# Optimization experiments

Measured on AMD Instinct MI355X. Metric: run time of the kernel, lower is better.

The kernel has to match this reference:

```python
import jax, jax.numpy as jnp
import numpy as np

N = 50000
E = 600000
D = 128
BN_EPS = 1e-5
GIN_EPS = 0.0  # init_eps=0, not learned


def setup_inputs() -> dict:
    key = jax.random.key(0)
    ks = jax.random.split(key, 8)
    x = jax.random.normal(ks[0], (N, D), dtype=jnp.float32)
    edge_index = jax.random.randint(ks[1], (2, E), 0, N, dtype=jnp.int64)
    s = 1.0 / np.sqrt(D)
    w1 = jax.random.uniform(ks[2], (D, D), jnp.float32, -s, s)
    b1 = jax.random.uniform(ks[3], (D,), jnp.float32, -s, s)
    w2 = jax.random.uniform(ks[4], (D, D), jnp.float32, -s, s)
    b2 = jax.random.uniform(ks[5], (D,), jnp.float32, -s, s)
    gamma = jnp.ones((D,), jnp.float32)
    beta = jnp.zeros((D,), jnp.float32)
    return {"x": x, "edge_index": edge_index, "w1": w1, "b1": b1,
            "w2": w2, "b2": b2, "gamma": gamma, "beta": beta}


def reference(x, edge_index, w1, b1, w2, b2, gamma, beta):
    src, dst = edge_index[0], edge_index[1]
    # GINConv sum aggregation: out[i] = sum_{(j,i) in E} x[j]
    agg = jax.ops.segment_sum(x[src], dst, num_segments=N)  # [N, D]
    h = (1.0 + GIN_EPS) * x + agg
    # 2-layer MLP (Linear-ReLU-Linear)
    h = jax.nn.relu(h @ w1 + b1)
    h = h @ w2 + b2
    # training-mode BatchNorm over nodes (biased variance)
    mean = jnp.mean(h, axis=0)
    var = jnp.var(h, axis=0)
    h = (h - mean) * jax.lax.rsqrt(var + BN_EPS) * gamma + beta
    h = jax.nn.relu(h)
    # residual (in_dim == out_dim); dropout p=0.0 -> identity
    return x + h
```

## Files before the change

### kernel.cpp

```cpp
#include <hip/hip_runtime.h>

#define NN 50000
#define EE 600000
#define DD 128
#define MAXDEG 64
#define NSLICE 32
#define EPT 4

typedef __attribute__((ext_vector_type(8))) short short8;
typedef __attribute__((ext_vector_type(4))) float f32x4;

static __device__ __forceinline__ unsigned short f2bf(float f) {
    unsigned int u = __float_as_uint(f);
    u += 0x7FFF + ((u >> 16) & 1);
    return (unsigned short)(u >> 16);
}
static __device__ __forceinline__ float bflo(unsigned int u) {
    return __uint_as_float(u << 16);
}
static __device__ __forceinline__ float bfhi(unsigned int u) {
    return __uint_as_float(u & 0xFFFF0000u);
}


__global__ __launch_bounds__(256) void k_prep(const float* __restrict__ w1,
                                              const float* __restrict__ w2,
                                              const float* __restrict__ x,
                                              const int* __restrict__ ei,
                                              int* __restrict__ cursor,
                                              unsigned short* __restrict__ srcPad,
                                              unsigned short* __restrict__ wt,
                                              unsigned int* __restrict__ xb) {
    int tid = blockIdx.x * 256 + threadIdx.x;
    if (tid < EE / EPT) {
        #pragma unroll
        for (int i = 0; i < EPT; ++i) {
            int e = tid + i * (EE / EPT);
            int s = ei[e];
            int d = ei[EE + e];
            int pos = atomicAdd(&cursor[d], 1);
            if (pos < MAXDEG) srcPad[(d << 6) + pos] = (unsigned short)s;
        }
    }
    if (tid < 32768) {
        int w = tid >> 14, idx = tid & 16383;
        int k = idx >> 7, n = idx & 127;
        const float* src = w ? w2 : w1;
        wt[w * 16384 + n * 128 + k] = f2bf(src[k * 128 + n]);
    }
    int xi = tid - 32768;
    if (xi >= 0 && xi < NN * DD / 2) {
        float2 v = ((const float2*)x)[xi];
        xb[xi] = (unsigned int)f2bf(v.x) | ((unsigned int)f2bf(v.y) << 16);
    }
}


__global__ __launch_bounds__(256) void k_agg(const unsigned int* __restrict__ xb,
                                             const int* __restrict__ cursor,
                                             const unsigned short* __restrict__ srcPad,
                                             unsigned int* __restrict__ h0) {
    int wave = (blockIdx.x * blockDim.x + threadIdx.x) >> 6;
    int lane = threadIdx.x & 63;
    if (wave >= NN) return;
    int cnt = cursor[wave];
    if (cnt > MAXDEG) cnt = MAXDEG;
    int sv = srcPad[(wave << 6) + lane];
    unsigned int self = xb[(wave << 6) + lane];
    float ax = bflo(self), ay = bfhi(self);
    int j = 0;
    for (; j + 8 <= cnt; j += 8) {
        int a0 = __shfl(sv, j, 64),     a1 = __shfl(sv, j + 1, 64);
        int a2 = __shfl(sv, j + 2, 64), a3 = __shfl(sv, j + 3, 64);
        int a4 = __shfl(sv, j + 4, 64), a5 = __shfl(sv, j + 5, 64);
        int a6 = __shfl(sv, j + 6, 64), a7 = __shfl(sv, j + 7, 64);
        unsigned int u0 = xb[(a0 << 6) + lane], u1 = xb[(a1 << 6) + lane];
        unsigned int u2 = xb[(a2 << 6) + lane], u3 = xb[(a3 << 6) + lane];
        unsigned int u4 = xb[(a4 << 6) + lane], u5 = xb[(a5 << 6) + lane];
        unsigned int u6 = xb[(a6 << 6) + lane], u7 = xb[(a7 << 6) + lane];
        ax += bflo(u0) + bflo(u1) + bflo(u2) + bflo(u3)
            + bflo(u4) + bflo(u5) + bflo(u6) + bflo(u7);
        ay += bfhi(u0) + bfhi(u1) + bfhi(u2) + bfhi(u3)
            + bfhi(u4) + bfhi(u5) + bfhi(u6) + bfhi(u7);
    }
    for (; j + 4 <= cnt; j += 4) {
        int a0 = __shfl(sv, j, 64),     a1 = __shfl(sv, j + 1, 64);
        int a2 = __shfl(sv, j + 2, 64), a3 = __shfl(sv, j + 3, 64);
        unsigned int u0 = xb[(a0 << 6) + lane], u1 = xb[(a1 << 6) + lane];
        unsigned int u2 = xb[(a2 << 6) + lane], u3 = xb[(a3 << 6) + lane];
        ax += bflo(u0) + bflo(u1) + bflo(u2) + bflo(u3);
        ay += bfhi(u0) + bfhi(u1) + bfhi(u2) + bfhi(u3);
    }
    for (; j < cnt; ++j) {
        int s = __shfl(sv, j, 64);
        unsigned int u = xb[(s << 6) + lane];
        ax += bflo(u);
        ay += bfhi(u);
    }
    h0[(wave << 6) + lane] = (unsigned int)f2bf(ax) | ((unsigned int)f2bf(ay) << 16);
}


__global__ __launch_bounds__(256) void k_gemm(const unsigned short* __restrict__ A,
                                              const unsigned short* __restrict__ W,
                                              const float* __restrict__ bias,
                                              unsigned short* __restrict__ Cb,
                                              float* __restrict__ priv,
                                              int relu) {
    int wave = (blockIdx.x * 256 + threadIdx.x) >> 6;
    int lane = threadIdx.x & 63;
    int m = lane & 15, quad = lane >> 4;
    int row0 = wave * 32;
    if (row0 >= NN) return;

    short8 af[2][4];
    #pragma unroll
    for (int mt = 0; mt < 2; ++mt) {
        int gr = row0 + mt * 16 + m;
        #pragma unroll
        for (int kc = 0; kc < 4; ++kc)
            af[mt][kc] = (gr < NN) ? *(const short8*)&A[gr * 128 + kc * 32 + quad * 8]
                                   : (short8)0;
    }

    f32x4 acc[2][8];
    #pragma unroll
    for (int mt = 0; mt < 2; ++mt)
        #pragma unroll
        for (int i = 0; i < 8; ++i) acc[mt][i] = (f32x4)0.f;

    #pragma unroll
    for (int h = 0; h < 2; ++h) {
        short8 wf[4][4];
        #pragma unroll
        for (int nt = 0; nt < 4; ++nt)
            #pragma unroll
            for (int kc = 0; kc < 4; ++kc)
                wf[nt][kc] = *(const short8*)&W[(h * 64 + nt * 16 + m) * 128 + kc * 32 + quad * 8];
        #pragma unroll
        for (int kc = 0; kc < 4; ++kc)
            #pragma unroll
            for (int nt = 0; nt < 4; ++nt) {
                acc[0][h * 4 + nt] = __builtin_amdgcn_mfma_f32_16x16x32_bf16(af[0][kc], wf[nt][kc], acc[0][h * 4 + nt], 0, 0, 0);
                acc[1][h * 4 + nt] = __builtin_amdgcn_mfma_f32_16x16x32_bf16(af[1][kc], wf[nt][kc], acc[1][h * 4 + nt], 0, 0, 0);
            }
    }

    if (relu) {
        #pragma unroll
        for (int nt = 0; nt < 8; ++nt) {
            int col = nt * 16 + m;
            float bv = bias[col];
            #pragma unroll
            for (int mt = 0; mt < 2; ++mt)
                #pragma unroll
                for (int r = 0; r < 4; ++r) {
                    int gr = row0 + mt * 16 + quad * 4 + r;
                    if (gr < NN) Cb[gr * 128 + col] = f2bf(fmaxf(acc[mt][nt][r] + bv, 0.f));
                }
        }
    } else {
        float* myslice = priv + (wave & (NSLICE - 1)) * 2 * DD;
        #pragma unroll
        for (int nt = 0; nt < 8; ++nt) {
            int col = nt * 16 + m;
            float bv = bias[col];
            float s = 0.f, sq = 0.f;
            #pragma unroll
            for (int mt = 0; mt < 2; ++mt)
                #pragma unroll
                for (int r = 0; r < 4; ++r) {
                    int gr = row0 + mt * 16 + quad * 4 + r;
                    if (gr < NN) {
                        float v = acc[mt][nt][r] + bv;
                        Cb[gr * 128 + col] = f2bf(v);
                        s += v;
                        sq += v * v;
                    }
                }
            s  += __shfl_down(s, 32, 64);  sq += __shfl_down(sq, 32, 64);
            s  += __shfl_down(s, 16, 64);  sq += __shfl_down(sq, 16, 64);
            if (quad == 0) {
                atomicAdd(&myslice[col], s);
                atomicAdd(&myslice[DD + col], sq);
            }
        }
    }
}


__global__ __launch_bounds__(256) void k_final(const float* __restrict__ x,
                                               const unsigned int* __restrict__ h2,
                                               float* __restrict__ out,
                                               const float* __restrict__ priv,
                                               const float* __restrict__ gamma,
                                               const float* __restrict__ beta) {
    __shared__ float ssc[DD], ssh[DD];
    int t = threadIdx.x;
    if (t < DD) {
        float s = 0.f, sq = 0.f;
        #pragma unroll
        for (int sl = 0; sl < NSLICE; ++sl) {
            s  += priv[sl * 2 * DD + t];
            sq += priv[sl * 2 * DD + DD + t];
        }
        float mean = s * (1.0f / NN);
        float var = fmaxf(sq * (1.0f / NN) - mean * mean, 0.f);
        float sc = gamma[t] * rsqrtf(var + 1e-5f);
        ssc[t] = sc;
        ssh[t] = beta[t] - mean * sc;
    }
    __syncthreads();
    #pragma unroll
    for (int u = 0; u < 4; ++u) {
        int idx = blockIdx.x * 1024 + u * 256 + t;
        if (idx >= NN * DD / 4) return;
        int c0 = (idx & 31) * 4;
        unsigned int p0 = h2[2 * idx];
        unsigned int p1 = h2[2 * idx + 1];
        float4 xv = ((const float4*)x)[idx];
        float4 o;
        o.x = xv.x + fmaxf(fmaf(bflo(p0), ssc[c0 + 0], ssh[c0 + 0]), 0.f);
        o.y = xv.y + fmaxf(fmaf(bfhi(p0), ssc[c0 + 1], ssh[c0 + 1]), 0.f);
        o.z = xv.z + fmaxf(fmaf(bflo(p1), ssc[c0 + 2], ssh[c0 + 2]), 0.f);
        o.w = xv.w + fmaxf(fmaf(bfhi(p1), ssc[c0 + 3], ssh[c0 + 3]), 0.f);
        ((float4*)out)[idx] = o;
    }
}

extern "C" void kernel_launch(void* const* d_in, const int* in_sizes, int n_in,
                              void* d_out, int out_size, void* d_ws, size_t ws_size,
                              hipStream_t stream) {
    (void)in_sizes; (void)n_in; (void)out_size; (void)ws_size;
    const float* x     = (const float*)d_in[0];
    const int*   ei    = (const int*)d_in[1];
    const float* w1    = (const float*)d_in[2];
    const float* b1    = (const float*)d_in[3];
    const float* w2    = (const float*)d_in[4];
    const float* b2    = (const float*)d_in[5];
    const float* gamma = (const float*)d_in[6];
    const float* beta  = (const float*)d_in[7];
    float* out = (float*)d_out;

    char* wsb = (char*)d_ws;
    int*            cursor = (int*)(wsb);
    unsigned short* srcPad = (unsigned short*)(wsb + 0x40000);
    unsigned int*   xb     = (unsigned int*)(wsb + 0x680000);
    unsigned short* h1b    = (unsigned short*)xb;
    unsigned int*   h0w    = (unsigned int*)(wsb + 0x1300000);
    unsigned short* h0b    = (unsigned short*)h0w;
    unsigned short* h2b    = (unsigned short*)h0w;
    unsigned int*   h2w    = (unsigned int*)h0w;
    unsigned short* wt     = (unsigned short*)(wsb + 0x1F80000);
    float*          priv   = (float*)(wsb + 0x1FA0000);

    (void)hipMemsetAsync(cursor, 0, NN * sizeof(int), stream);
    (void)hipMemsetAsync(priv, 0, NSLICE * 2 * DD * sizeof(float), stream);

    k_prep<<<(32768 + NN * DD / 2 + 255) / 256, 256, 0, stream>>>(w1, w2, x, ei, cursor, srcPad, wt, xb);
    k_agg<<<(NN * 64 + 255) / 256, 256, 0, stream>>>(xb, cursor, srcPad, h0w);
    k_gemm<<<(NN + 127) / 128, 256, 0, stream>>>(h0b, wt, b1, h1b, nullptr, 1);
    k_gemm<<<(NN + 127) / 128, 256, 0, stream>>>(h1b, wt + 16384, b2, h2b, priv, 0);
    k_final<<<(NN * DD / 4 + 1023) / 1024, 256, 0, stream>>>(x, h2w, out, priv, gamma, beta);
}
```

Baseline: 192.9 us.

## Fuse the two MLP GEMMs into one kernel with the hidden tile kept in LDS

Replaces the two separate GEMM launches with one k_mlp kernel. Each block computes 64 rows of the first linear plus ReLU, stores the bf16 hidden tile in padded shared memory, then runs the second GEMM and the BatchNorm statistics from it. This removes the global write and re-read of the intermediate activation and one launch. It also merges the two memsets into one by moving priv next to cursor, and raises EPT to 8. In exchange, each wave now handles 16 rows instead of 32, so every W fragment loaded feeds fewer MFMAs.

```diff
diff --git a/kernel.cpp b/kernel.cpp
--- a/kernel.cpp
+++ b/kernel.cpp
@@ -3,9 +3,10 @@
 #define NN 50000
 #define EE 600000
 #define DD 128
+#define LDSTR 136
 #define MAXDEG 64
 #define NSLICE 32
-#define EPT 4
+#define EPT 8
 
 typedef __attribute__((ext_vector_type(8))) short short8;
 typedef __attribute__((ext_vector_type(4))) float f32x4;
@@ -101,34 +102,28 @@
 }
 
 
-__global__ __launch_bounds__(256) void k_gemm(const unsigned short* __restrict__ A,
-                                              const unsigned short* __restrict__ W,
-                                              const float* __restrict__ bias,
-                                              unsigned short* __restrict__ Cb,
-                                              float* __restrict__ priv,
-                                              int relu) {
-    int wave = (blockIdx.x * 256 + threadIdx.x) >> 6;
-    int lane = threadIdx.x & 63;
+__global__ __launch_bounds__(256) void k_mlp(const unsigned short* A,
+                                             const unsigned short* __restrict__ wt,
+                                             const float* __restrict__ b1,
+                                             const float* __restrict__ b2,
+                                             unsigned short* C,
+                                             float* __restrict__ priv) {
+    __shared__ __align__(16) unsigned short H1s[64 * LDSTR];
+    int t = threadIdx.x;
+    int lane = t & 63, wid = t >> 6;
     int m = lane & 15, quad = lane >> 4;
-    int row0 = wave * 32;
-    if (row0 >= NN) return;
-
-    short8 af[2][4];
-    #pragma unroll
-    for (int mt = 0; mt < 2; ++mt) {
-        int gr = row0 + mt * 16 + m;
-        #pragma unroll
-        for (int kc = 0; kc < 4; ++kc)
-            af[mt][kc] = (gr < NN) ? *(const short8*)&A[gr * 128 + kc * 32 + quad * 8]
-                                   : (short8)0;
-    }
-
-    f32x4 acc[2][8];
-    #pragma unroll
-    for (int mt = 0; mt < 2; ++mt)
-        #pragma unroll
-        for (int i = 0; i < 8; ++i) acc[mt][i] = (f32x4)0.f;
-
+    int row0 = blockIdx.x * 64 + wid * 16;
+
+    int gra = row0 + m;
+    short8 af[4];
+    #pragma unroll
+    for (int kc = 0; kc < 4; ++kc)
+        af[kc] = (gra < NN) ? *(const short8*)&A[gra * 128 + kc * 32 + quad * 8]
+                            : (short8)0;
+
+    f32x4 acc[8];
+    #pragma unroll
+    for (int i = 0; i < 8; ++i) acc[i] = (f32x4)0.f;
     #pragma unroll
     for (int h = 0; h < 2; ++h) {
         short8 wf[4][4];
@@ -136,54 +131,67 @@
         for (int nt = 0; nt < 4; ++nt)
             #pragma unroll
             for (int kc = 0; kc < 4; ++kc)
-                wf[nt][kc] = *(const short8*)&W[(h * 64 + nt * 16 + m) * 128 + kc * 32 + quad * 8];
+                wf[nt][kc] = *(const short8*)&wt[(h * 64 + nt * 16 + m) * 128 + kc * 32 + quad * 8];
         #pragma unroll
         for (int kc = 0; kc < 4; ++kc)
             #pragma unroll
-            for (int nt = 0; nt < 4; ++nt) {
-                acc[0][h * 4 + nt] = __builtin_amdgcn_mfma_f32_16x16x32_bf16(af[0][kc], wf[nt][kc], acc[0][h * 4 + nt], 0, 0, 0);
-                acc[1][h * 4 + nt] = __builtin_amdgcn_mfma_f32_16x16x32_bf16(af[1][kc], wf[nt][kc], acc[1][h * 4 + nt], 0, 0, 0);
+            for (int nt = 0; nt < 4; ++nt)
+                acc[h * 4 + nt] = __builtin_amdgcn_mfma_f32_16x16x32_bf16(af[kc], wf[nt][kc], acc[h * 4 + nt], 0, 0, 0);
+    }
+
+    #pragma unroll
+    for (int nt = 0; nt < 8; ++nt) {
+        int col = nt * 16 + m;
+        float bv = b1[col];
+        #pragma unroll
+        for (int r = 0; r < 4; ++r)
+            H1s[(wid * 16 + quad * 4 + r) * LDSTR + col] = f2bf(fmaxf(acc[nt][r] + bv, 0.f));
+    }
+    __syncthreads();
+
+    short8 af2[4];
+    #pragma unroll
+    for (int kc = 0; kc < 4; ++kc)
+        af2[kc] = *(const short8*)&H1s[(wid * 16 + m) * LDSTR + kc * 32 + quad * 8];
+
+    #pragma unroll
+    for (int i = 0; i < 8; ++i) acc[i] = (f32x4)0.f;
+    #pragma unroll
+    for (int h = 0; h < 2; ++h) {
+        short8 wf[4][4];
+        #pragma unroll
+        for (int nt = 0; nt < 4; ++nt)
+            #pragma unroll
+            for (int kc = 0; kc < 4; ++kc)
+                wf[nt][kc] = *(const short8*)&wt[16384 + (h * 64 + nt * 16 + m) * 128 + kc * 32 + quad * 8];
+        #pragma unroll
+        for (int kc = 0; kc < 4; ++kc)
+            #pragma unroll
+            for (int nt = 0; nt < 4; ++nt)
+                acc[h * 4 + nt] = __builtin_amdgcn_mfma_f32_16x16x32_bf16(af2[kc], wf[nt][kc], acc[h * 4 + nt], 0, 0, 0);
+    }
+
+    float* myslice = priv + ((blockIdx.x * 4 + wid) & (NSLICE - 1)) * 2 * DD;
+    #pragma unroll
+    for (int nt = 0; nt < 8; ++nt) {
+        int col = nt * 16 + m;
+        float bv = b2[col];
+        float s = 0.f, sq = 0.f;
+        #pragma unroll
+        for (int r = 0; r < 4; ++r) {
+            int gr = row0 + quad * 4 + r;
+            if (gr < NN) {
+                float v = acc[nt][r] + bv;
+                C[gr * 128 + col] = f2bf(v);
+                s += v;
+                sq += v * v;
             }
-    }
-
-    if (relu) {
-        #pragma unroll
-        for (int nt = 0; nt < 8; ++nt) {
-            int col = nt * 16 + m;
-            float bv = bias[col];
-            #pragma unroll
-            for (int mt = 0; mt < 2; ++mt)
-                #pragma unroll
-                for (int r = 0; r < 4; ++r) {
-                    int gr = row0 + mt * 16 + quad * 4 + r;
-                    if (gr < NN) Cb[gr * 128 + col] = f2bf(fmaxf(acc[mt][nt][r] + bv, 0.f));
-                }
-        }
-    } else {
-        float* myslice = priv + (wave & (NSLICE - 1)) * 2 * DD;
-        #pragma unroll
-        for (int nt = 0; nt < 8; ++nt) {
-            int col = nt * 16 + m;
-            float bv = bias[col];
-            float s = 0.f, sq = 0.f;
-            #pragma unroll
-            for (int mt = 0; mt < 2; ++mt)
-                #pragma unroll
-                for (int r = 0; r < 4; ++r) {
-                    int gr = row0 + mt * 16 + quad * 4 + r;
-                    if (gr < NN) {
-                        float v = acc[mt][nt][r] + bv;
-                        Cb[gr * 128 + col] = f2bf(v);
-                        s += v;
-                        sq += v * v;
-                    }
-                }
-            s  += __shfl_down(s, 32, 64);  sq += __shfl_down(sq, 32, 64);
-            s  += __shfl_down(s, 16, 64);  sq += __shfl_down(sq, 16, 64);
-            if (quad == 0) {
-                atomicAdd(&myslice[col], s);
-                atomicAdd(&myslice[DD + col], sq);
-            }
+        }
+        s  += __shfl_down(s, 32, 64);  sq += __shfl_down(sq, 32, 64);
+        s  += __shfl_down(s, 16, 64);  sq += __shfl_down(sq, 16, 64);
+        if (quad == 0) {
+            atomicAdd(&myslice[col], s);
+            atomicAdd(&myslice[DD + col], sq);
         }
     }
 }
@@ -244,22 +252,19 @@
 
     char* wsb = (char*)d_ws;
     int*            cursor = (int*)(wsb);
+    float*          priv   = (float*)(wsb + 0x31000);
     unsigned short* srcPad = (unsigned short*)(wsb + 0x40000);
     unsigned int*   xb     = (unsigned int*)(wsb + 0x680000);
-    unsigned short* h1b    = (unsigned short*)xb;
     unsigned int*   h0w    = (unsigned int*)(wsb + 0x1300000);
     unsigned short* h0b    = (unsigned short*)h0w;
     unsigned short* h2b    = (unsigned short*)h0w;
     unsigned int*   h2w    = (unsigned int*)h0w;
     unsigned short* wt     = (unsigned short*)(wsb + 0x1F80000);
-    float*          priv   = (float*)(wsb + 0x1FA0000);
-
-    (void)hipMemsetAsync(cursor, 0, NN * sizeof(int), stream);
-    (void)hipMemsetAsync(priv, 0, NSLICE * 2 * DD * sizeof(float), stream);
+
+    (void)hipMemsetAsync(wsb, 0, 0x39000, stream);
 
     k_prep<<<(32768 + NN * DD / 2 + 255) / 256, 256, 0, stream>>>(w1, w2, x, ei, cursor, srcPad, wt, xb);
     k_agg<<<(NN * 64 + 255) / 256, 256, 0, stream>>>(xb, cursor, srcPad, h0w);
-    k_gemm<<<(NN + 127) / 128, 256, 0, stream>>>(h0b, wt, b1, h1b, nullptr, 1);
-    k_gemm<<<(NN + 127) / 128, 256, 0, stream>>>(h1b, wt + 16384, b2, h2b, priv, 0);
+    k_mlp<<<(NN + 63) / 64, 256, 0, stream>>>(h0b, wt, b1, b2, h2b, priv);
     k_final<<<(NN * DD / 4 + 1023) / 1024, 256, 0, stream>>>(x, h2w, out, priv, gamma, beta);
 }
```

Result: slower. 199.8 us (+3.6%).

## Fuse all stages into one cooperative persistent kernel with grid syncs

Applied to the files above, without the earlier changes.

Replaces the memset plus five kernel launches with a single cooperative kernel that runs every stage (zeroing, CSR build, bf16 conversion, aggregation, both GEMMs, BatchNorm finalize) in grid-stride loops separated by grid.sync(). The aim is to remove launch and inter-kernel gaps. In exchange the stages run on a capped persistent grid, which may reduce parallelism and latency hiding, and each grid barrier has its own cost. Intermediate buffers are no longer aliased, and the old multi-kernel path is kept as a fallback.

```diff
diff --git a/kernel.cpp b/kernel.cpp
--- a/kernel.cpp
+++ b/kernel.cpp
@@ -1,11 +1,14 @@
 #include <hip/hip_runtime.h>
+#include <hip/hip_cooperative_groups.h>
+
+namespace cg = cooperative_groups;
 
 #define NN 50000
 #define EE 600000
 #define DD 128
 #define MAXDEG 64
 #define NSLICE 32
-#define EPT 4
+#define EPT 8
 
 typedef __attribute__((ext_vector_type(8))) short short8;
 typedef __attribute__((ext_vector_type(4))) float f32x4;
@@ -23,50 +26,96 @@
 }
 
 
-__global__ __launch_bounds__(256) void k_prep(const float* __restrict__ w1,
-                                              const float* __restrict__ w2,
-                                              const float* __restrict__ x,
-                                              const int* __restrict__ ei,
-                                              int* __restrict__ cursor,
-                                              unsigned short* __restrict__ srcPad,
-                                              unsigned short* __restrict__ wt,
-                                              unsigned int* __restrict__ xb) {
-    int tid = blockIdx.x * 256 + threadIdx.x;
-    if (tid < EE / EPT) {
-        #pragma unroll
-        for (int i = 0; i < EPT; ++i) {
-            int e = tid + i * (EE / EPT);
-            int s = ei[e];
-            int d = ei[EE + e];
-            int pos = atomicAdd(&cursor[d], 1);
-            if (pos < MAXDEG) srcPad[(d << 6) + pos] = (unsigned short)s;
-        }
-    }
-    if (tid < 32768) {
-        int w = tid >> 14, idx = tid & 16383;
-        int k = idx >> 7, n = idx & 127;
-        const float* src = w ? w2 : w1;
-        wt[w * 16384 + n * 128 + k] = f2bf(src[k * 128 + n]);
-    }
-    int xi = tid - 32768;
-    if (xi >= 0 && xi < NN * DD / 2) {
-        float2 v = ((const float2*)x)[xi];
-        xb[xi] = (unsigned int)f2bf(v.x) | ((unsigned int)f2bf(v.y) << 16);
-    }
-}
-
-
-__global__ __launch_bounds__(256) void k_agg(const unsigned int* __restrict__ xb,
-                                             const int* __restrict__ cursor,
-                                             const unsigned short* __restrict__ srcPad,
-                                             unsigned int* __restrict__ h0) {
-    int wave = (blockIdx.x * blockDim.x + threadIdx.x) >> 6;
-    int lane = threadIdx.x & 63;
-    if (wave >= NN) return;
-    int cnt = cursor[wave];
+static __device__ __forceinline__ void gemm32(const unsigned short* __restrict__ A,
+                                              const unsigned short* __restrict__ W,
+                                              const float* __restrict__ bias,
+                                              unsigned short* __restrict__ C,
+                                              float* __restrict__ priv,
+                                              int lane, int row0, int relu, int unit) {
+    int m = lane & 15, quad = lane >> 4;
+    short8 af[2][4];
+    #pragma unroll
+    for (int mt = 0; mt < 2; ++mt) {
+        int gr = row0 + mt * 16 + m;
+        #pragma unroll
+        for (int kc = 0; kc < 4; ++kc)
+            af[mt][kc] = (gr < NN) ? *(const short8*)&A[gr * 128 + kc * 32 + quad * 8]
+                                   : (short8)0;
+    }
+    f32x4 acc[2][8];
+    #pragma unroll
+    for (int mt = 0; mt < 2; ++mt)
+        #pragma unroll
+        for (int i = 0; i < 8; ++i) acc[mt][i] = (f32x4)0.f;
+
+    #pragma unroll
+    for (int h = 0; h < 2; ++h) {
+        short8 wf[4][4];
+        #pragma unroll
+        for (int nt = 0; nt < 4; ++nt)
+            #pragma unroll
+            for (int kc = 0; kc < 4; ++kc)
+                wf[nt][kc] = *(const short8*)&W[(h * 64 + nt * 16 + m) * 128 + kc * 32 + quad * 8];
+        #pragma unroll
+        for (int kc = 0; kc < 4; ++kc)
+            #pragma unroll
+            for (int nt = 0; nt < 4; ++nt) {
+                acc[0][h * 4 + nt] = __builtin_amdgcn_mfma_f32_16x16x32_bf16(af[0][kc], wf[nt][kc], acc[0][h * 4 + nt], 0, 0, 0);
+                acc[1][h * 4 + nt] = __builtin_amdgcn_mfma_f32_16x16x32_bf16(af[1][kc], wf[nt][kc], acc[1][h * 4 + nt], 0, 0, 0);
+            }
+    }
+
+    if (relu) {
+        #pragma unroll
+        for (int nt = 0; nt < 8; ++nt) {
+            int col = nt * 16 + m;
+            float bv = bias[col];
+            #pragma unroll
+            for (int mt = 0; mt < 2; ++mt)
+                #pragma unroll
+                for (int r = 0; r < 4; ++r) {
+                    int gr = row0 + mt * 16 + quad * 4 + r;
+                    if (gr < NN) C[gr * 128 + col] = f2bf(fmaxf(acc[mt][nt][r] + bv, 0.f));
+                }
+        }
+    } else {
+        float* myslice = priv + (unit & (NSLICE - 1)) * 2 * DD;
+        #pragma unroll
+        for (int nt = 0; nt < 8; ++nt) {
+            int col = nt * 16 + m;
+            float bv = bias[col];
+            float s = 0.f, sq = 0.f;
+            #pragma unroll
+            for (int mt = 0; mt < 2; ++mt)
+                #pragma unroll
+                for (int r = 0; r < 4; ++r) {
+                    int gr = row0 + mt * 16 + quad * 4 + r;
+                    if (gr < NN) {
+                        float v = acc[mt][nt][r] + bv;
+                        C[gr * 128 + col] = f2bf(v);
+                        s += v;
+                        sq += v * v;
+                    }
+                }
+            s  += __shfl_down(s, 32, 64);  sq += __shfl_down(sq, 32, 64);
+            s  += __shfl_down(s, 16, 64);  sq += __shfl_down(sq, 16, 64);
+            if (quad == 0) {
+                atomicAdd(&myslice[col], s);
+                atomicAdd(&myslice[DD + col], sq);
+            }
+        }
+    }
+}
+
+static __device__ __forceinline__ void agg_node(int node, int lane,
+                                                const unsigned int* __restrict__ xb,
+                                                const int* __restrict__ cursor,
+                                                const unsigned short* __restrict__ srcPad,
+                                                unsigned int* __restrict__ h0) {
+    int cnt = cursor[node];
     if (cnt > MAXDEG) cnt = MAXDEG;
-    int sv = srcPad[(wave << 6) + lane];
-    unsigned int self = xb[(wave << 6) + lane];
+    int sv = srcPad[(node << 6) + lane];
+    unsigned int self = xb[(node << 6) + lane];
     float ax = bflo(self), ay = bfhi(self);
     int j = 0;
     for (; j + 8 <= cnt; j += 8) {
@@ -97,9 +146,144 @@
         ax += bflo(u);
         ay += bfhi(u);
     }
-    h0[(wave << 6) + lane] = (unsigned int)f2bf(ax) | ((unsigned int)f2bf(ay) << 16);
-}
-
+    h0[(node << 6) + lane] = (unsigned int)f2bf(ax) | ((unsigned int)f2bf(ay) << 16);
+}
+
+
+__global__ __launch_bounds__(256) void k_all(const float* __restrict__ x,
+                                             const int* __restrict__ ei,
+                                             const float* __restrict__ w1,
+                                             const float* __restrict__ b1,
+                                             const float* __restrict__ w2,
+                                             const float* __restrict__ b2,
+                                             const float* __restrict__ gamma,
+                                             const float* __restrict__ beta,
+                                             float* __restrict__ out,
+                                             char* __restrict__ wsb) {
+    cg::grid_group grid = cg::this_grid();
+    int*            cursor = (int*)wsb;
+    float*          priv   = (float*)(wsb + 0x31000);
+    unsigned short* srcPad = (unsigned short*)(wsb + 0x40000);
+    unsigned int*   xb     = (unsigned int*)(wsb + 0x680000);
+    unsigned int*   h0w    = (unsigned int*)(wsb + 0x1300000);
+    unsigned short* h1b    = (unsigned short*)(wsb + 0x1F80000);
+    unsigned int*   h2w    = (unsigned int*)(wsb + 0x2C00000);
+    unsigned short* wt     = (unsigned short*)(wsb + 0x3880000);
+    const unsigned short* h0b = (const unsigned short*)h0w;
+    unsigned short*       h2b = (unsigned short*)h2w;
+
+    int nth = gridDim.x * 256;
+    int nwave = nth >> 6;
+    int tid = blockIdx.x * 256 + threadIdx.x;
+    int lane = tid & 63;
+    int gwave = tid >> 6;
+
+    for (int i = tid; i < NN; i += nth) cursor[i] = 0;
+    for (int i = tid; i < NSLICE * 2 * DD; i += nth) priv[i] = 0.f;
+    grid.sync();
+
+    for (int e = tid; e < EE; e += nth) {
+        int s = ei[e];
+        int d = ei[EE + e];
+        int pos = atomicAdd(&cursor[d], 1);
+        if (pos < MAXDEG) srcPad[(d << 6) + pos] = (unsigned short)s;
+    }
+    for (int i = tid; i < 32768; i += nth) {
+        int w = i >> 14, idx = i & 16383;
+        int k = idx >> 7, n = idx & 127;
+        const float* src = w ? w2 : w1;
+        wt[w * 16384 + n * 128 + k] = f2bf(src[k * 128 + n]);
+    }
+    for (int xi = tid; xi < NN * DD / 2; xi += nth) {
+        float2 v = ((const float2*)x)[xi];
+        xb[xi] = (unsigned int)f2bf(v.x) | ((unsigned int)f2bf(v.y) << 16);
+    }
+    grid.sync();
+
+    for (int node = gwave; node < NN; node += nwave)
+        agg_node(node, lane, xb, cursor, srcPad, h0w);
+    grid.sync();
+
+    for (int unit = gwave; unit * 32 < NN; unit += nwave)
+        gemm32(h0b, wt, b1, h1b, nullptr, lane, unit * 32, 1, unit);
+    grid.sync();
+
+    for (int unit = gwave; unit * 32 < NN; unit += nwave)
+        gemm32(h1b, wt + 16384, b2, h2b, priv, lane, unit * 32, 0, unit);
+    grid.sync();
+
+    __shared__ float ssc[DD], ssh[DD];
+    int t = threadIdx.x;
+    if (t < DD) {
+        float s = 0.f, sq = 0.f;
+        #pragma unroll
+        for (int sl = 0; sl < NSLICE; ++sl) {
+            s  += priv[sl * 2 * DD + t];
+            sq += priv[sl * 2 * DD + DD + t];
+        }
+        float mean = s * (1.0f / NN);
+        float var = fmaxf(sq * (1.0f / NN) - mean * mean, 0.f);
+        float sc = gamma[t] * rsqrtf(var + 1e-5f);
+        ssc[t] = sc;
+        ssh[t] = beta[t] - mean * sc;
+    }
+    __syncthreads();
+    for (int idx = tid; idx < NN * DD / 4; idx += nth) {
+        int c0 = (idx & 31) * 4;
+        unsigned int p0 = h2w[2 * idx];
+        unsigned int p1 = h2w[2 * idx + 1];
+        float4 xv = ((const float4*)x)[idx];
+        float4 o;
+        o.x = xv.x + fmaxf(fmaf(bflo(p0), ssc[c0 + 0], ssh[c0 + 0]), 0.f);
+        o.y = xv.y + fmaxf(fmaf(bfhi(p0), ssc[c0 + 1], ssh[c0 + 1]), 0.f);
+        o.z = xv.z + fmaxf(fmaf(bflo(p1), ssc[c0 + 2], ssh[c0 + 2]), 0.f);
+        o.w = xv.w + fmaxf(fmaf(bfhi(p1), ssc[c0 + 3], ssh[c0 + 3]), 0.f);
+        ((float4*)out)[idx] = o;
+    }
+}
+
+
+__global__ __launch_bounds__(256) void k_prep(const float* __restrict__ w1,
+                                              const float* __restrict__ w2,
+                                              const float* __restrict__ x,
+                                              const int* __restrict__ ei,
+                                              int* __restrict__ cursor,
+                                              unsigned short* __restrict__ srcPad,
+                                              unsigned short* __restrict__ wt,
+                                              unsigned int* __restrict__ xb) {
+    int tid = blockIdx.x * 256 + threadIdx.x;
+    if (tid < EE / EPT) {
+        #pragma unroll
+        for (int i = 0; i < EPT; ++i) {
+            int e = tid + i * (EE / EPT);
+            int s = ei[e];
+            int d = ei[EE + e];
+            int pos = atomicAdd(&cursor[d], 1);
+            if (pos < MAXDEG) srcPad[(d << 6) + pos] = (unsigned short)s;
+        }
+    }
+    if (tid < 32768) {
+        int w = tid >> 14, idx = tid & 16383;
+        int k = idx >> 7, n = idx & 127;
+        const float* src = w ? w2 : w1;
+        wt[w * 16384 + n * 128 + k] = f2bf(src[k * 128 + n]);
+    }
+    int xi = tid - 32768;
+    if (xi >= 0 && xi < NN * DD / 2) {
+        float2 v = ((const float2*)x)[xi];
+        xb[xi] = (unsigned int)f2bf(v.x) | ((unsigned int)f2bf(v.y) << 16);
+    }
+}
+
+__global__ __launch_bounds__(256) void k_agg(const unsigned int* __restrict__ xb,
+                                             const int* __restrict__ cursor,
+                                             const unsigned short* __restrict__ srcPad,
+                                             unsigned int* __restrict__ h0) {
+    int wave = (blockIdx.x * blockDim.x + threadIdx.x) >> 6;
+    int lane = threadIdx.x & 63;
+    if (wave >= NN) return;
+    agg_node(wave, lane, xb, cursor, srcPad, h0);
+}
 
 __global__ __launch_bounds__(256) void k_gemm(const unsigned short* __restrict__ A,
                                               const unsigned short* __restrict__ W,
@@ -109,85 +293,10 @@
                                               int relu) {
     int wave = (blockIdx.x * 256 + threadIdx.x) >> 6;
     int lane = threadIdx.x & 63;
-    int m = lane & 15, quad = lane >> 4;
     int row0 = wave * 32;
     if (row0 >= NN) return;
-
-    short8 af[2][4];
-    #pragma unroll
-    for (int mt = 0; mt < 2; ++mt) {
-        int gr = row0 + mt * 16 + m;
-        #pragma unroll
-        for (int kc = 0; kc < 4; ++kc)
-            af[mt][kc] = (gr < NN) ? *(const short8*)&A[gr * 128 + kc * 32 + quad * 8]
-                                   : (short8)0;
-    }
-
-    f32x4 acc[2][8];
-    #pragma unroll
-    for (int mt = 0; mt < 2; ++mt)
-        #pragma unroll
-        for (int i = 0; i < 8; ++i) acc[mt][i] = (f32x4)0.f;
-
-    #pragma unroll
-    for (int h = 0; h < 2; ++h) {
-        short8 wf[4][4];
-        #pragma unroll
-        for (int nt = 0; nt < 4; ++nt)
-            #pragma unroll
-            for (int kc = 0; kc < 4; ++kc)
-                wf[nt][kc] = *(const short8*)&W[(h * 64 + nt * 16 + m) * 128 + kc * 32 + quad * 8];
-        #pragma unroll
-        for (int kc = 0; kc < 4; ++kc)
-            #pragma unroll
-            for (int nt = 0; nt < 4; ++nt) {
-                acc[0][h * 4 + nt] = __builtin_amdgcn_mfma_f32_16x16x32_bf16(af[0][kc], wf[nt][kc], acc[0][h * 4 + nt], 0, 0, 0);
-                acc[1][h * 4 + nt] = __builtin_amdgcn_mfma_f32_16x16x32_bf16(af[1][kc], wf[nt][kc], acc[1][h * 4 + nt], 0, 0, 0);
-            }
-    }
-
-    if (relu) {
-        #pragma unroll
-        for (int nt = 0; nt < 8; ++nt) {
-            int col = nt * 16 + m;
-            float bv = bias[col];
-            #pragma unroll
-            for (int mt = 0; mt < 2; ++mt)
-                #pragma unroll
-                for (int r = 0; r < 4; ++r) {
-                    int gr = row0 + mt * 16 + quad * 4 + r;
-                    if (gr < NN) Cb[gr * 128 + col] = f2bf(fmaxf(acc[mt][nt][r] + bv, 0.f));
-                }
-        }
-    } else {
-        float* myslice = priv + (wave & (NSLICE - 1)) * 2 * DD;
-        #pragma unroll
-        for (int nt = 0; nt < 8; ++nt) {
-            int col = nt * 16 + m;
-            float bv = bias[col];
-            float s = 0.f, sq = 0.f;
-            #pragma unroll
-            for (int mt = 0; mt < 2; ++mt)
-                #pragma unroll
-                for (int r = 0; r < 4; ++r) {
-                    int gr = row0 + mt * 16 + quad * 4 + r;
-                    if (gr < NN) {
-                        float v = acc[mt][nt][r] + bv;
-                        Cb[gr * 128 + col] = f2bf(v);
-                        s += v;
-                        sq += v * v;
-                    }
-                }
-            s  += __shfl_down(s, 32, 64);  sq += __shfl_down(sq, 32, 64);
-            s  += __shfl_down(s, 16, 64);  sq += __shfl_down(sq, 16, 64);
-            if (quad == 0) {
-                atomicAdd(&myslice[col], s);
-                atomicAdd(&myslice[DD + col], sq);
-            }
-        }
-    }
-}
-
+    gemm32(A, W, bias, Cb, priv, lane, row0, relu, wave);
+}
 
 __global__ __launch_bounds__(256) void k_final(const float* __restrict__ x,
                                                const unsigned int* __restrict__ h2,
@@ -241,22 +350,42 @@
     const float* gamma = (const float*)d_in[6];
     const float* beta  = (const float*)d_in[7];
     float* out = (float*)d_out;
-
-    char* wsb = (char*)d_ws;
-    int*            cursor = (int*)(wsb);
+    char* wsb  = (char*)d_ws;
+
+    int*            cursor = (int*)wsb;
+    float*          priv   = (float*)(wsb + 0x31000);
     unsigned short* srcPad = (unsigned short*)(wsb + 0x40000);
     unsigned int*   xb     = (unsigned int*)(wsb + 0x680000);
-    unsigned short* h1b    = (unsigned short*)xb;
     unsigned int*   h0w    = (unsigned int*)(wsb + 0x1300000);
-    unsigned short* h0b    = (unsigned short*)h0w;
-    unsigned short* h2b    = (unsigned short*)h0w;
-    unsigned int*   h2w    = (unsigned int*)h0w;
-    unsigned short* wt     = (unsigned short*)(wsb + 0x1F80000);
-    float*          priv   = (float*)(wsb + 0x1FA0000);
-
-    (void)hipMemsetAsync(cursor, 0, NN * sizeof(int), stream);
-    (void)hipMemsetAsync(priv, 0, NSLICE * 2 * DD * sizeof(float), stream);
-
+    unsigned short* h1b    = (unsigned short*)(wsb + 0x1F80000);
+    unsigned int*   h2w    = (unsigned int*)(wsb + 0x2C00000);
+    unsigned short* wt     = (unsigned short*)(wsb + 0x3880000);
+    const unsigned short* h0b = (const unsigned short*)h0w;
+    unsigned short*       h2b = (unsigned short*)h2w;
+
+    bool coop_ok = false;
+    int dev = 0;
+    if (hipGetDevice(&dev) == hipSuccess) {
+        int has_coop = 0;
+        if (hipDeviceGetAttribute(&has_coop, hipDeviceAttributeCooperativeLaunch, dev) == hipSuccess
+            && has_coop) {
+            int blocks_per_cu = 0;
+            if (hipOccupancyMaxActiveBlocksPerMultiprocessor(
+                    &blocks_per_cu, reinterpret_cast<const void*>(&k_all), 256, 0) == hipSuccess
+                && blocks_per_cu > 0) {
+                int nb = blocks_per_cu * 256;
+                if (nb > 2048) nb = 2048;
+                void* args[] = {(void*)&x, (void*)&ei, (void*)&w1, (void*)&b1, (void*)&w2,
+                                (void*)&b2, (void*)&gamma, (void*)&beta, (void*)&out, (void*)&wsb};
+                if (hipLaunchCooperativeKernel(reinterpret_cast<const void*>(&k_all),
+                                               dim3(nb), dim3(256), args, 0, stream) == hipSuccess)
+                    coop_ok = true;
+            }
+        }
+    }
+    if (coop_ok) return;
+
+    (void)hipMemsetAsync(wsb, 0, 0x39000, stream);
     k_prep<<<(32768 + NN * DD / 2 + 255) / 256, 256, 0, stream>>>(w1, w2, x, ei, cursor, srcPad, wt, xb);
     k_agg<<<(NN * 64 + 255) / 256, 256, 0, stream>>>(xb, cursor, srcPad, h0w);
     k_gemm<<<(NN + 127) / 128, 256, 0, stream>>>(h0b, wt, b1, h1b, nullptr, 1);
```

Result: faster. 182.9 us (-5.1%).
